# Optimization experiments

Hardware: AMD Instinct MI355X
Metric: run time of the kernel (lower is better)

Reference implementation:

```python
import jax, jax.numpy as jnp
import numpy as np

DN = ('NCHW', 'OIHW', 'NCHW')

def conv(x, w, b=None, stride=1, pad=0):
    y = jax.lax.conv_general_dilated(x, w, (stride, stride), [(pad, pad), (pad, pad)],
                                     dimension_numbers=DN)
    return y if b is None else y + b[None, :, None, None]

def conv_t(x, w, b, stride=2, pad=1):
    # PyTorch ConvTranspose2d: w is (in, out, kh, kw); equivalent to an
    # input-dilated conv with spatially flipped, in/out-swapped kernel.
    k = w.shape[2]
    w2 = jnp.flip(w, (2, 3)).transpose(1, 0, 2, 3)
    p = k - 1 - pad
    y = jax.lax.conv_general_dilated(x, w2, (1, 1), [(p, p), (p, p)],
                                     lhs_dilation=(stride, stride), dimension_numbers=DN)
    return y + b[None, :, None, None]

def res_block(x, wa, wb):
    h = conv(jax.nn.relu(x), wa, None, 1, 1)   # 3x3, no bias
    h = conv(jax.nn.relu(h), wb, None, 1, 0)   # 1x1, no bias
    return x + h

def vq(x, codebook):
    B, C, H, W = x.shape
    xf = x.transpose(0, 2, 3, 1).reshape(-1, C)                      # (N, D)
    d = ((xf * xf).sum(-1, keepdims=True)
         - 2.0 * xf @ codebook.T
         + (codebook * codebook).sum(-1)[None, :])
    idx = jnp.argmin(d, axis=1)                                      # (N,)
    q = jnp.take(codebook, idx, axis=0)                              # gather (N, D)
    return q.reshape(B, H, W, C).transpose(0, 3, 1, 2)

def setup_inputs() -> dict:
    key = jax.random.key(0)
    ks = jax.random.split(key, 16)
    r = lambda i, shape: jax.random.normal(ks[i], shape, jnp.float32) * 0.05
    K, D = 512, 64
    return {
        'x': jax.random.normal(ks[0], (32, 1, 256, 256), jnp.float32),
        'w_e1': r(1, (32, 1, 4, 4)),   'b_e1': jnp.zeros((32,), jnp.float32),
        'w_e2': r(2, (64, 32, 4, 4)),  'b_e2': jnp.zeros((64,), jnp.float32),
        'w_er1a': r(3, (32, 64, 3, 3)), 'w_er1b': r(4, (64, 32, 1, 1)),
        'w_er2a': r(5, (32, 64, 3, 3)), 'w_er2b': r(6, (64, 32, 1, 1)),
        'w_pre': r(7, (D, 64, 1, 1)),  'b_pre': jnp.zeros((D,), jnp.float32),
        'codebook': jax.random.uniform(ks[8], (K, D), jnp.float32, -1.0 / K, 1.0 / K),
        'w_d1': r(9, (64, D, 3, 3)),   'b_d1': jnp.zeros((64,), jnp.float32),
        'w_dr1a': r(10, (32, 64, 3, 3)), 'w_dr1b': r(11, (64, 32, 1, 1)),
        'w_dr2a': r(12, (32, 64, 3, 3)), 'w_dr2b': r(13, (64, 32, 1, 1)),
        'w_t1': r(14, (64, 32, 4, 4)), 'b_t1': jnp.zeros((32,), jnp.float32),
        'w_t2': r(15, (32, 1, 4, 4)),  'b_t2': jnp.zeros((1,), jnp.float32),
    }

def reference(x, w_e1, b_e1, w_e2, b_e2, w_er1a, w_er1b, w_er2a, w_er2b,
              w_pre, b_pre, codebook, w_d1, b_d1, w_dr1a, w_dr1b,
              w_dr2a, w_dr2b, w_t1, b_t1, w_t2, b_t2):
    # Encoder
    h = jax.nn.relu(conv(x, w_e1, b_e1, 2, 1))     # (B,32,128,128)
    h = conv(h, w_e2, b_e2, 2, 1)                  # (B,64,64,64)
    h = res_block(h, w_er1a, w_er1b)
    h = res_block(h, w_er2a, w_er2b)
    # pre-VQ 1x1 conv
    h = conv(h, w_pre, b_pre, 1, 0)                # (B,64,64,64)
    # Vector quantization
    q = vq(h, codebook)
    # Decoder
    d = conv(q, w_d1, b_d1, 1, 1)
    d = res_block(d, w_dr1a, w_dr1b)
    d = res_block(d, w_dr2a, w_dr2b)
    d = jax.nn.relu(conv_t(d, w_t1, b_t1))         # (B,32,128,128)
    d = conv_t(d, w_t2, b_t2)                      # (B,1,256,256)
    return d
```

## Files before the change

### kernel.cpp

```cpp
#include <hip/hip_runtime.h>
#include <hip/hip_bf16.h>


__device__ __forceinline__ float rp_elem(const float* __restrict__ src,
                                         int i, int COUT, int CIN, int KK)
{
    const int co = i % COUT;
    const int t  = i / COUT;
    const int kk = t % KK;
    const int ci = t / KK;
    return src[(co * CIN + ci) * KK + kk];
}

__global__ __launch_bounds__(256) void repack_all(
    const float* __restrict__ e1,  const float* __restrict__ e2,
    const float* __restrict__ er1a, const float* __restrict__ er1b,
    const float* __restrict__ er2a, const float* __restrict__ er2b,
    const float* __restrict__ pre, const float* __restrict__ d1,
    const float* __restrict__ dr1a, const float* __restrict__ dr1b,
    const float* __restrict__ dr2a, const float* __restrict__ dr2b,
    const float* __restrict__ t1, const float* __restrict__ cb,
    float* __restrict__ WR)
{
    const int idx = blockIdx.x * 256 + threadIdx.x;
    if (idx >= 221696) return;
    float v;
    if      (idx < 512)    v = rp_elem(e1,   idx,          32,  1, 16);
    else if (idx < 33280)  v = rp_elem(e2,   idx - 512,    64, 32, 16);
    else if (idx < 51712)  v = rp_elem(er1a, idx - 33280,  32, 64,  9);
    else if (idx < 53760)  v = rp_elem(er1b, idx - 51712,  64, 32,  1);
    else if (idx < 72192)  v = rp_elem(er2a, idx - 53760,  32, 64,  9);
    else if (idx < 74240)  v = rp_elem(er2b, idx - 72192,  64, 32,  1);
    else if (idx < 78336)  v = rp_elem(pre,  idx - 74240,  64, 64,  1);
    else if (idx < 115200) v = rp_elem(d1,   idx - 78336,  64, 64,  9);
    else if (idx < 133632) v = rp_elem(dr1a, idx - 115200, 32, 64,  9);
    else if (idx < 135680) v = rp_elem(dr1b, idx - 133632, 64, 32,  1);
    else if (idx < 154112) v = rp_elem(dr2a, idx - 135680, 32, 64,  9);
    else if (idx < 156160) v = rp_elem(dr2b, idx - 154112, 64, 32,  1);
    else if (idx < 188928) {
        const int i  = idx - 156160;
        const int co = i & 31;
        const int q  = (i >> 5) & 3;
        const int k2 = (i >> 7) & 127;
        const int pr = i >> 14;
        const int pc = q >> 1, tb = q & 1;
        const int ci = k2 >> 1, ta = k2 & 1;
        const int kh = (1 - pr) + 2 * ta, kw = (1 - pc) + 2 * tb;
        v = t1[((ci * 32 + co) * 4 + kh) * 4 + kw];
    } else {
        const int i = idx - 188928;
        const int code = i & 511;
        const int dim  = i >> 9;
        v = cb[code * 64 + dim];
    }
    WR[idx] = v;
}

__global__ __launch_bounds__(256) void vq_prep_ee(
    const float* __restrict__ cb, float* __restrict__ ee)
{
    const int k = blockIdx.x * 256 + threadIdx.x;
    const float* __restrict__ cp = cb + (size_t)k * 64;
    float s = 0.0f;
#pragma unroll
    for (int i = 0; i < 64; i++) s = fmaf(cp[i], cp[i], s);
    ee[k] = s;
}

template<int CTOT, int CPB, int CIN, int K, int S, int PAD,
         bool RELU_IN, bool HAS_BIAS, bool RESID, bool RELU_OUT>
__global__ __launch_bounds__(256) void conv_gemm(
    const float* __restrict__ in, const float* __restrict__ wr,
    const float* __restrict__ bias, const float* __restrict__ resid,
    float* __restrict__ out,
    int H, int W, int OH, int OW)
{
    constexpr int KK  = K * K;
    constexpr int CIC = (K == 1) ? 8 : 1;
    constexpr int TS  = (K == 4) ? 2 : 1;
    constexpr int KC  = CIC * KK / TS;
    constexpr int NCH = (CIN * TS) / CIC;
    constexpr int NT  = 256;
    constexpr int CPTHD = CPB / 4;
    __shared__ __align__(16) float As[2][KC * NT];

    const int tid = threadIdx.x;
    const int tpx = tid & 63;
    const int tco = __builtin_amdgcn_readfirstlane(tid >> 6);
    const int co0 = blockIdx.y * CPB + tco * CPTHD;

    const int ohow = OH * OW;
    const int n_st = blockIdx.x * NT + tid;
    const int b_st = n_st / ohow;
    const int hw_s = n_st % ohow;
    const int ih0 = (hw_s / OW) * S - PAD;
    const int iw0 = (hw_s % OW) * S - PAD;
    const float* __restrict__ inb = in + (size_t)b_st * CIN * H * W;

    float acc[CPTHD][4];
#pragma unroll
    for (int c = 0; c < CPTHD; c++) {
        const float bz = HAS_BIAS ? bias[co0 + c] : 0.0f;
#pragma unroll
        for (int q = 0; q < 4; q++) acc[c][q] = bz;
    }

    float pf[KC];
    auto stage_load = [&](int ch) {
#pragma unroll
        for (int t = 0; t < KC; t++) {
            int ci, kh, kw;
            if constexpr (K == 1) {
                ci = ch * 8 + t; kh = 0; kw = 0;
            } else if constexpr (K == 3) {
                ci = ch; kh = t / 3; kw = t % 3;
            } else {
                ci = ch >> 1;
                const int kk = ((ch & 1) << 3) + t;
                kh = kk >> 2; kw = kk & 3;
            }
            const int ih = ih0 + kh, iw = iw0 + kw;
            float v = 0.0f;
            if (ih >= 0 && ih < H && iw >= 0 && iw < W)
                v = inb[(size_t)ci * H * W + ih * W + iw];
            if (RELU_IN) v = fmaxf(v, 0.0f);
            pf[t] = v;
        }
    };

    stage_load(0);
#pragma unroll
    for (int t = 0; t < KC; t++) As[0][t * NT + tid] = pf[t];
    __syncthreads();

#pragma unroll 2
    for (int c = 0; c < NCH; c++) {
        const int cur = c & 1;
        if (c + 1 < NCH) stage_load(c + 1);

#pragma unroll
        for (int t = 0; t < KC; t++) {
            const float4 a4 = *(const float4*)(As[cur] + t * NT + tpx * 4);
            const float* __restrict__ wk =
                wr + (size_t)(c * KC + t) * CTOT + co0;
#pragma unroll
            for (int cc = 0; cc < CPTHD; cc++) {
                const float w = wk[cc];
                acc[cc][0] = fmaf(a4.x, w, acc[cc][0]);
                acc[cc][1] = fmaf(a4.y, w, acc[cc][1]);
                acc[cc][2] = fmaf(a4.z, w, acc[cc][2]);
                acc[cc][3] = fmaf(a4.w, w, acc[cc][3]);
            }
        }

        if (c + 1 < NCH) {
#pragma unroll
            for (int t = 0; t < KC; t++) As[1 - cur][t * NT + tid] = pf[t];
        }
        __syncthreads();
    }

    const int n_c  = blockIdx.x * NT + tpx * 4;
    const int b_c  = n_c / ohow;
    const int hw_c = n_c % ohow;
    float* __restrict__ op = out + (size_t)b_c * CTOT * ohow + hw_c;
    const float* __restrict__ rp =
        RESID ? (resid + (size_t)b_c * CTOT * ohow + hw_c) : nullptr;
#pragma unroll
    for (int c = 0; c < CPTHD; c++) {
        const size_t off = (size_t)(co0 + c) * ohow;
        float4 r = make_float4(acc[c][0], acc[c][1], acc[c][2], acc[c][3]);
        if (RESID) {
            const float4 rv = *(const float4*)(rp + off);
            r.x += rv.x; r.y += rv.y; r.z += rv.z; r.w += rv.w;
        }
        if (RELU_OUT) {
            r.x = fmaxf(r.x, 0.f); r.y = fmaxf(r.y, 0.f);
            r.z = fmaxf(r.z, 0.f); r.w = fmaxf(r.w, 0.f);
        }
        *(float4*)(op + off) = r;
    }
}

__global__ __launch_bounds__(512, 4) void res_tile(
    const float* __restrict__ in, const float* __restrict__ wr1,
    const float* __restrict__ wr2, float* __restrict__ out)
{
    __shared__ __align__(16) float S[13824];

    const int tid = threadIdx.x;
    const int p   = tid & 127;
    const int cog = __builtin_amdgcn_readfirstlane(tid >> 7);
    const int a   = p >> 5;
    const int c0  = (p & 31) * 2;

    const int n0   = blockIdx.x * 256;
    const int b    = n0 >> 12;
    const int row0 = (n0 & 4095) >> 6;
    const float* __restrict__ inb = in + (size_t)b * 64 * 4096;

    float4 pf4[7];
    auto stage_issue = [&](int half) {
#pragma unroll
        for (int m = 0; m < 7; m++) {
            const int f4 = m * 512 + tid;
            float4 v = make_float4(0.f, 0.f, 0.f, 0.f);
            if (f4 < 3456) {
                const int ci  = f4 / 108;
                const int rem = f4 - ci * 108;
                const int r6  = rem / 18;
                const int c4  = rem - r6 * 18;
                const int ih  = row0 + r6 - 1;
                if (ih >= 0 && ih < 64 && c4 >= 1 && c4 <= 16)
                    v = *(const float4*)(inb + (size_t)(half * 32 + ci) * 4096
                                         + ih * 64 + (c4 * 4 - 4));
            }
            pf4[m] = v;
        }
    };
    auto stage_commit = [&]() {
#pragma unroll
        for (int m = 0; m < 7; m++) {
            const int f4 = m * 512 + tid;
            if (f4 < 3456) {
                float4 v = pf4[m];
                v.x = fmaxf(v.x, 0.f); v.y = fmaxf(v.y, 0.f);
                v.z = fmaxf(v.z, 0.f); v.w = fmaxf(v.w, 0.f);
                *(float4*)(S + f4 * 4) = v;
            }
        }
    };

    const int co1 = cog * 8;
    float acc1[8][2];
#pragma unroll
    for (int c = 0; c < 8; c++) { acc1[c][0] = 0.0f; acc1[c][1] = 0.0f; }

    auto conv1_half = [&](int h) {
#pragma unroll 2
        for (int c = 0; c < 32; c++) {
            const float* __restrict__ wb =
                wr1 + (size_t)((h * 32 + c) * 9) * 32 + co1;
#pragma unroll
            for (int kh = 0; kh < 3; kh++) {
                const float* __restrict__ tp =
                    S + c * 432 + (a + kh) * 72 + 4 + c0;
                const float2 L = *(const float2*)(tp - 2);
                const float2 M = *(const float2*)(tp);
                const float2 R = *(const float2*)(tp + 2);
                const float xm = L.y;
                const float x0 = M.x;
                const float x1 = M.y;
                const float x2 = R.x;
                const float* __restrict__ wk = wb + (size_t)(kh * 3) * 32;
#pragma unroll
                for (int cc = 0; cc < 8; cc++) {
                    const float w = wk[cc];
                    acc1[cc][0] = fmaf(xm, w, acc1[cc][0]);
                    acc1[cc][1] = fmaf(x0, w, acc1[cc][1]);
                }
#pragma unroll
                for (int cc = 0; cc < 8; cc++) {
                    const float w = wk[32 + cc];
                    acc1[cc][0] = fmaf(x0, w, acc1[cc][0]);
                    acc1[cc][1] = fmaf(x1, w, acc1[cc][1]);
                }
#pragma unroll
                for (int cc = 0; cc < 8; cc++) {
                    const float w = wk[64 + cc];
                    acc1[cc][0] = fmaf(x1, w, acc1[cc][0]);
                    acc1[cc][1] = fmaf(x2, w, acc1[cc][1]);
                }
            }
        }
    };

    stage_issue(0);
    stage_commit();
    __syncthreads();
    stage_issue(1);
    conv1_half(0);
    __syncthreads();
    stage_commit();
    __syncthreads();
    conv1_half(1);
    __syncthreads();

#pragma unroll
    for (int cc = 0; cc < 8; cc++)
        *(float2*)(S + (co1 + cc) * 256 + p * 2) =
            make_float2(acc1[cc][0], acc1[cc][1]);
    __syncthreads();

    const int co2 = cog * 16;
    float acc2[16][2];
#pragma unroll
    for (int c = 0; c < 16; c++) { acc2[c][0] = 0.0f; acc2[c][1] = 0.0f; }

#pragma unroll 4
    for (int k = 0; k < 32; k++) {
        float2 m2 = *(const float2*)(S + k * 256 + p * 2);
        m2.x = fmaxf(m2.x, 0.f);
        m2.y = fmaxf(m2.y, 0.f);
        const float* __restrict__ wk = wr2 + (size_t)k * 64 + co2;
#pragma unroll
        for (int cc = 0; cc < 16; cc++) {
            const float w = wk[cc];
            acc2[cc][0] = fmaf(m2.x, w, acc2[cc][0]);
            acc2[cc][1] = fmaf(m2.y, w, acc2[cc][1]);
        }
    }

    const int hw = (n0 & 4095) + p * 2;
    const float* __restrict__ rp = inb + hw;
    float* __restrict__ op = out + (size_t)b * 64 * 4096 + hw;
#pragma unroll
    for (int cc = 0; cc < 16; cc++) {
        const size_t off = (size_t)(co2 + cc) * 4096;
        const float2 rv = *(const float2*)(rp + off);
        *(float2*)(op + off) =
            make_float2(acc2[cc][0] + rv.x, acc2[cc][1] + rv.y);
    }
}

__global__ __launch_bounds__(512, 4) void conv3_tile(
    const float* __restrict__ in, const float* __restrict__ wr,
    const float* __restrict__ bias, float* __restrict__ out)
{
    __shared__ __align__(16) float S[13824];

    const int tid = threadIdx.x;
    const int p   = tid & 127;
    const int cog = __builtin_amdgcn_readfirstlane(tid >> 7);
    const int a   = p >> 5;
    const int c0  = (p & 31) * 2;

    const int n0   = blockIdx.x * 256;
    const int b    = n0 >> 12;
    const int row0 = (n0 & 4095) >> 6;
    const float* __restrict__ inb = in + (size_t)b * 64 * 4096;

    float4 pf4[7];
    auto stage_issue = [&](int half) {
#pragma unroll
        for (int m = 0; m < 7; m++) {
            const int f4 = m * 512 + tid;
            float4 v = make_float4(0.f, 0.f, 0.f, 0.f);
            if (f4 < 3456) {
                const int ci  = f4 / 108;
                const int rem = f4 - ci * 108;
                const int r6  = rem / 18;
                const int c4  = rem - r6 * 18;
                const int ih  = row0 + r6 - 1;
                if (ih >= 0 && ih < 64 && c4 >= 1 && c4 <= 16)
                    v = *(const float4*)(inb + (size_t)(half * 32 + ci) * 4096
                                         + ih * 64 + (c4 * 4 - 4));
            }
            pf4[m] = v;
        }
    };
    auto stage_commit = [&]() {
#pragma unroll
        for (int m = 0; m < 7; m++) {
            const int f4 = m * 512 + tid;
            if (f4 < 3456) *(float4*)(S + f4 * 4) = pf4[m];
        }
    };

    const int co1 = cog * 16;
    float acc[16][2];
#pragma unroll
    for (int cc = 0; cc < 16; cc++) {
        const float bz = bias[co1 + cc];
        acc[cc][0] = bz; acc[cc][1] = bz;
    }

    auto conv_half = [&](int h) {
#pragma unroll 2
        for (int c = 0; c < 32; c++) {
            const float* __restrict__ wb =
                wr + (size_t)((h * 32 + c) * 9) * 64 + co1;
#pragma unroll
            for (int kh = 0; kh < 3; kh++) {
                const float* __restrict__ tp =
                    S + c * 432 + (a + kh) * 72 + 4 + c0;
                const float2 L = *(const float2*)(tp - 2);
                const float2 M = *(const float2*)(tp);
                const float2 R = *(const float2*)(tp + 2);
                const float xm = L.y;
                const float x0 = M.x;
                const float x1 = M.y;
                const float x2 = R.x;
                const float* __restrict__ wk = wb + (size_t)(kh * 3) * 64;
#pragma unroll
                for (int cc = 0; cc < 16; cc++) {
                    const float w = wk[cc];
                    acc[cc][0] = fmaf(xm, w, acc[cc][0]);
                    acc[cc][1] = fmaf(x0, w, acc[cc][1]);
                }
#pragma unroll
                for (int cc = 0; cc < 16; cc++) {
                    const float w = wk[64 + cc];
                    acc[cc][0] = fmaf(x0, w, acc[cc][0]);
                    acc[cc][1] = fmaf(x1, w, acc[cc][1]);
                }
#pragma unroll
                for (int cc = 0; cc < 16; cc++) {
                    const float w = wk[128 + cc];
                    acc[cc][0] = fmaf(x1, w, acc[cc][0]);
                    acc[cc][1] = fmaf(x2, w, acc[cc][1]);
                }
            }
        }
    };

    stage_issue(0);
    stage_commit();
    __syncthreads();
    stage_issue(1);
    conv_half(0);
    __syncthreads();
    stage_commit();
    __syncthreads();
    conv_half(1);

    const int hw = (n0 & 4095) + p * 2;
    float* __restrict__ op = out + (size_t)b * 64 * 4096 + hw;
#pragma unroll
    for (int cc = 0; cc < 16; cc++)
        *(float2*)(op + (size_t)(co1 + cc) * 4096) =
            make_float2(acc[cc][0], acc[cc][1]);
}

__global__ __launch_bounds__(512, 4) void conv4s2_tile(
    const float* __restrict__ in, const float* __restrict__ wr,
    const float* __restrict__ bias, float* __restrict__ out)
{
    __shared__ __align__(16) float S[13056];

    const int tid = threadIdx.x;
    const int p   = tid & 63;
    const int cog = __builtin_amdgcn_readfirstlane(tid >> 6);
    const int a   = p >> 5;
    const int c0  = (p & 31) * 2;

    const int n0   = blockIdx.x * 128;
    const int b    = n0 >> 12;
    const int row0 = (n0 & 4095) >> 6;
    const float* __restrict__ inb = in + (size_t)b * 32 * 16384;

    float4 pf4[7];
    auto stage_issue = [&](int half) {
#pragma unroll
        for (int m = 0; m < 7; m++) {
            const int f4 = m * 512 + tid;
            float4 v = make_float4(0.f, 0.f, 0.f, 0.f);
            if (f4 < 3264) {
                const int ci  = f4 / 204;
                const int rem = f4 - ci * 204;
                const int r6  = rem / 34;
                const int s   = rem - r6 * 34;
                const int ih  = 2 * row0 - 1 + r6;
                if (ih >= 0 && ih < 128 && s >= 1 && s <= 32)
                    v = *(const float4*)(inb + (size_t)(half * 16 + ci) * 16384
                                         + ih * 128 + (s - 1) * 4);
            }
            pf4[m] = v;
        }
    };
    auto stage_commit = [&]() {
#pragma unroll
        for (int m = 0; m < 7; m++) {
            const int f4 = m * 512 + tid;
            if (f4 < 3264) *(float4*)(S + f4 * 4) = pf4[m];
        }
    };

    const int co1 = cog * 8;
    float acc[8][2];
#pragma unroll
    for (int cc = 0; cc < 8; cc++) {
        const float bz = bias[co1 + cc];
        acc[cc][0] = bz; acc[cc][1] = bz;
    }

    auto conv_half = [&](int h) {
#pragma unroll 2
        for (int c = 0; c < 16; c++) {
            const float* __restrict__ wb =
                wr + (size_t)((h * 16 + c) * 16) * 64 + co1;
#pragma unroll
            for (int kh = 0; kh < 4; kh++) {
                const float* __restrict__ tp =
                    S + c * 816 + (2 * a + kh) * 136 + 2 * c0 + 2;
                const float2 E0 = *(const float2*)(tp);
                const float2 E1 = *(const float2*)(tp + 2);
                const float2 E2 = *(const float2*)(tp + 4);
                const float2 E3 = *(const float2*)(tp + 6);
                const float x0 = E0.y, x1 = E1.x, x2 = E1.y;
                const float x3 = E2.x, x4 = E2.y, x5 = E3.x;
                const float* __restrict__ wk = wb + (size_t)(kh * 4) * 64;
#pragma unroll
                for (int cc = 0; cc < 8; cc++) {
                    const float w = wk[cc];
                    acc[cc][0] = fmaf(x0, w, acc[cc][0]);
                    acc[cc][1] = fmaf(x2, w, acc[cc][1]);
                }
#pragma unroll
                for (int cc = 0; cc < 8; cc++) {
                    const float w = wk[64 + cc];
                    acc[cc][0] = fmaf(x1, w, acc[cc][0]);
                    acc[cc][1] = fmaf(x3, w, acc[cc][1]);
                }
#pragma unroll
                for (int cc = 0; cc < 8; cc++) {
                    const float w = wk[128 + cc];
                    acc[cc][0] = fmaf(x2, w, acc[cc][0]);
                    acc[cc][1] = fmaf(x4, w, acc[cc][1]);
                }
#pragma unroll
                for (int cc = 0; cc < 8; cc++) {
                    const float w = wk[192 + cc];
                    acc[cc][0] = fmaf(x3, w, acc[cc][0]);
                    acc[cc][1] = fmaf(x5, w, acc[cc][1]);
                }
            }
        }
    };

    stage_issue(0);
    stage_commit();
    __syncthreads();
    stage_issue(1);
    conv_half(0);
    __syncthreads();
    stage_commit();
    __syncthreads();
    conv_half(1);

    const int hw = (n0 & 4095) + p * 2;
    float* __restrict__ op = out + (size_t)b * 64 * 4096 + hw;
#pragma unroll
    for (int cc = 0; cc < 8; cc++)
        *(float2*)(op + (size_t)(co1 + cc) * 4096) =
            make_float2(acc[cc][0], acc[cc][1]);
}

__global__ __launch_bounds__(256) void convt_gemm2(
    const float* __restrict__ in, const float* __restrict__ wr,
    const float* __restrict__ bias, float* __restrict__ out)
{
    constexpr int NT = 256;
    __shared__ __align__(16) float As[2][12 * NT];

    const int tid = threadIdx.x;
    const int tpx = tid & 63;
    const int tco = __builtin_amdgcn_readfirstlane(tid >> 6);
    const int pr = blockIdx.y & 1;
    const int cg = blockIdx.y >> 1;
    const int co0 = cg * 16 + tco * 4;

    const int n_st = blockIdx.x * NT + tid;
    const int b = n_st >> 12;
    const int i_st = (n_st & 4095) >> 6;
    const int j_st = n_st & 63;
    const float* __restrict__ inb = in + (size_t)b * 64 * 4096;

    float acc[4][4][2];
#pragma unroll
    for (int c = 0; c < 4; c++) {
        const float bz = bias[co0 + c];
#pragma unroll
        for (int p = 0; p < 4; p++) {
            acc[c][p][0] = bz;
            acc[c][p][1] = bz;
        }
    }

    const float* __restrict__ wpr = wr + (size_t)pr * 128 * 4 * 32;

    float pf[12];
    auto stage_load = [&](int ch) {
#pragma unroll
        for (int t = 0; t < 4; t++) {
            const int k2 = ch * 4 + t;
            const int ci = k2 >> 1;
            const int ta = k2 & 1;
            const int ih = i_st + pr - ta;
            const bool rok = (ih >= 0) && (ih < 64);
            const float* __restrict__ row = inb + (size_t)ci * 4096 + ih * 64;
#pragma unroll
            for (int m = 0; m < 3; m++) {
                const int iw = j_st + m - 1;
                float v = 0.0f;
                if (rok && iw >= 0 && iw < 64) v = row[iw];
                pf[t * 3 + m] = v;
            }
        }
    };

    stage_load(0);
#pragma unroll
    for (int t = 0; t < 12; t++) As[0][t * NT + tid] = pf[t];
    __syncthreads();

#pragma unroll 2
    for (int ch = 0; ch < 32; ch++) {
        const int cur = ch & 1;
        if (ch + 1 < 32) stage_load(ch + 1);

#pragma unroll
        for (int t = 0; t < 4; t++) {
            float4 a[3];
#pragma unroll
            for (int m = 0; m < 3; m++)
                a[m] = *(const float4*)(As[cur] + (t * 3 + m) * NT + tpx * 4);
            const float* __restrict__ wk =
                wpr + (size_t)(ch * 4 + t) * 4 * 32 + co0;
#pragma unroll
            for (int tb = 0; tb < 2; tb++) {
#pragma unroll
                for (int pc = 0; pc < 2; pc++) {
                    const int q = pc * 2 + tb;
                    const int m = pc - tb + 1;
                    const float* __restrict__ wt = wk + q * 32;
                    const float vx = a[m].x, vy = a[m].y,
                                vz = a[m].z, vw = a[m].w;
#pragma unroll
                    for (int c = 0; c < 4; c++) {
                        const float w = wt[c];
                        acc[c][0][pc] = fmaf(vx, w, acc[c][0][pc]);
                        acc[c][1][pc] = fmaf(vy, w, acc[c][1][pc]);
                        acc[c][2][pc] = fmaf(vz, w, acc[c][2][pc]);
                        acc[c][3][pc] = fmaf(vw, w, acc[c][3][pc]);
                    }
                }
            }
        }

        if (ch + 1 < 32) {
#pragma unroll
            for (int t = 0; t < 12; t++) As[1 - cur][t * NT + tid] = pf[t];
        }
        __syncthreads();
    }

    const int n_c = blockIdx.x * NT + tpx * 4;
    const int i_c = (n_c & 4095) >> 6;
    const int j_c = n_c & 63;
    const int oh = 2 * i_c + pr;
    float* __restrict__ ob =
        out + (size_t)b * 32 * 16384 + (size_t)oh * 128 + 2 * j_c;
#pragma unroll
    for (int c = 0; c < 4; c++) {
        float* __restrict__ o = ob + (size_t)(co0 + c) * 16384;
        const float4 v0 = make_float4(
            fmaxf(acc[c][0][0], 0.f), fmaxf(acc[c][0][1], 0.f),
            fmaxf(acc[c][1][0], 0.f), fmaxf(acc[c][1][1], 0.f));
        const float4 v1 = make_float4(
            fmaxf(acc[c][2][0], 0.f), fmaxf(acc[c][2][1], 0.f),
            fmaxf(acc[c][3][0], 0.f), fmaxf(acc[c][3][1], 0.f));
        *(float4*)o = v0;
        *(float4*)(o + 4) = v1;
    }
}

__global__ __launch_bounds__(256) void convt2_quad(
    const float* __restrict__ in, const float* __restrict__ w,
    const float* __restrict__ bias, float* __restrict__ out, int B)
{
    const int IH = 128, IW = 128, CIN = 32, OW = 256;
    const int j = threadIdx.x & 127;
    const int i = (blockIdx.x << 1) + (threadIdx.x >> 7);
    const int b = blockIdx.y;

    const float* __restrict__ inb = in + (size_t)b * CIN * IH * IW;
    const float bz = bias[0];
    float a00 = bz, a01 = bz, a10 = bz, a11 = bz;

    const bool okm = (i > 0);
    const bool okp = (i < IH - 1);
    const bool olm = (j > 0);
    const bool olp = (j < IW - 1);

#pragma unroll 4
    for (int ci = 0; ci < CIN; ci++) {
        const float* __restrict__ p = inb + ((size_t)ci * IH + i) * IW + j;
        const float* __restrict__ wp = w + ci * 16;
        const float vmm = (okm && olm) ? p[-IW - 1] : 0.f;
        const float vm0 = okm ? p[-IW] : 0.f;
        const float vmp = (okm && olp) ? p[-IW + 1] : 0.f;
        const float v0m = olm ? p[-1] : 0.f;
        const float v00 = p[0];
        const float v0p = olp ? p[1] : 0.f;
        const float vpm = (okp && olm) ? p[IW - 1] : 0.f;
        const float vp0 = okp ? p[IW] : 0.f;
        const float vpp = (okp && olp) ? p[IW + 1] : 0.f;
        a00 = fmaf(v00, wp[1 * 4 + 1], a00);
        a00 = fmaf(v0m, wp[1 * 4 + 3], a00);
        a00 = fmaf(vm0, wp[3 * 4 + 1], a00);
        a00 = fmaf(vmm, wp[3 * 4 + 3], a00);
        a01 = fmaf(v0p, wp[1 * 4 + 0], a01);
        a01 = fmaf(v00, wp[1 * 4 + 2], a01);
        a01 = fmaf(vmp, wp[3 * 4 + 0], a01);
        a01 = fmaf(vm0, wp[3 * 4 + 2], a01);
        a10 = fmaf(vp0, wp[0 * 4 + 1], a10);
        a10 = fmaf(vpm, wp[0 * 4 + 3], a10);
        a10 = fmaf(v00, wp[2 * 4 + 1], a10);
        a10 = fmaf(v0m, wp[2 * 4 + 3], a10);
        a11 = fmaf(vpp, wp[0 * 4 + 0], a11);
        a11 = fmaf(vp0, wp[0 * 4 + 2], a11);
        a11 = fmaf(v0p, wp[2 * 4 + 0], a11);
        a11 = fmaf(v00, wp[2 * 4 + 2], a11);
    }

    float* __restrict__ outb = out + (size_t)b * 256 * 256;
    ((float2*)(outb + (size_t)(2 * i) * OW))[j] = make_float2(a00, a01);
    ((float2*)(outb + (size_t)(2 * i + 1) * OW))[j] = make_float2(a10, a11);
}

__global__ __launch_bounds__(256) void vq_gemm(
    const float* __restrict__ h,
    const float* __restrict__ cb,
    const float* __restrict__ cbT,
    const float* __restrict__ ee,
    float* __restrict__ q)
{
    __shared__ __align__(16) float As[64 * 128];
    __shared__ float xx_sh[128];
    __shared__ float pd[4 * 128];
    __shared__ int   pk[4 * 128];
    __shared__ int   bidx_sh[128];

    const int tid = threadIdx.x;
    const int tpx = tid & 63;
    const int w = __builtin_amdgcn_readfirstlane(tid >> 6);
    const int n0 = blockIdx.x * 128;
    const int b  = n0 >> 12;
    const int hw0 = n0 & 4095;

    const float* __restrict__ hb = h + (size_t)b * 64 * 4096 + hw0;
#pragma unroll
    for (int m = 0; m < 32; m++) {
        const int idx = m * 256 + tid;
        const int k = idx >> 7, p = idx & 127;
        As[idx] = hb[(size_t)k * 4096 + p];
    }
    __syncthreads();

    if (tid < 128) {
        float s = 0.0f;
#pragma unroll
        for (int i = 0; i < 64; i++) {
            const float v = As[i * 128 + tid];
            s = fmaf(v, v, s);
        }
        xx_sh[tid] = s;
    }
    __syncthreads();

    const float xx0 = xx_sh[tpx * 2];
    const float xx1 = xx_sh[tpx * 2 + 1];
    const int cwave = w * 128;

    float best0 = 3.402823466e+38f, best1 = 3.402823466e+38f;
    int bk0 = 0, bk1 = 0;

#pragma unroll 1
    for (int ch = 0; ch < 16; ch++) {
        const int cbase = cwave + ch * 8;
        float acc[8][2];
#pragma unroll
        for (int c = 0; c < 8; c++) { acc[c][0] = 0.0f; acc[c][1] = 0.0f; }

#pragma unroll 8
        for (int k = 0; k < 64; k++) {
            const float2 a2 = *(const float2*)(As + k * 128 + tpx * 2);
            const float* __restrict__ wk = cbT + (size_t)k * 512 + cbase;
#pragma unroll
            for (int c = 0; c < 8; c++) {
                const float wv = wk[c];
                acc[c][0] = fmaf(a2.x, wv, acc[c][0]);
                acc[c][1] = fmaf(a2.y, wv, acc[c][1]);
            }
        }
        const float* __restrict__ eep = ee + cbase;
#pragma unroll
        for (int c = 0; c < 8; c++) {
            const float eec = eep[c];
            const float d0 = xx0 - 2.0f * acc[c][0] + eec;
            const float d1 = xx1 - 2.0f * acc[c][1] + eec;
            if (d0 < best0) { best0 = d0; bk0 = cbase + c; }
            if (d1 < best1) { best1 = d1; bk1 = cbase + c; }
        }
    }

    pd[w * 128 + tpx * 2]     = best0;
    pd[w * 128 + tpx * 2 + 1] = best1;
    pk[w * 128 + tpx * 2]     = bk0;
    pk[w * 128 + tpx * 2 + 1] = bk1;
    __syncthreads();

    if (tid < 128) {
        float bd = pd[tid]; int bk = pk[tid];
#pragma unroll
        for (int ww = 1; ww < 4; ww++) {
            const float od = pd[ww * 128 + tid];
            if (od < bd) { bd = od; bk = pk[ww * 128 + tid]; }
        }
        bidx_sh[tid] = bk;
    }
    __syncthreads();

    {
        const int p  = tid & 127;
        const int d0 = (tid >> 7) * 32;
        const int bk = bidx_sh[p];
        const float4* __restrict__ cp4 = (const float4*)(cb + (size_t)bk * 64 + d0);
        float* __restrict__ qb = q + ((size_t)b * 64 + d0) * 4096 + hw0 + p;
#pragma unroll
        for (int i = 0; i < 8; i++) {
            const float4 v = cp4[i];
            qb[(size_t)(4 * i + 0) * 4096] = v.x;
            qb[(size_t)(4 * i + 1) * 4096] = v.y;
            qb[(size_t)(4 * i + 2) * 4096] = v.z;
            qb[(size_t)(4 * i + 3) * 4096] = v.w;
        }
    }
}

extern "C" void kernel_launch(void* const* d_in, const int* in_sizes, int n_in,
                              void* d_out, int out_size, void* d_ws, size_t ws_size,
                              hipStream_t stream) {
    const float* x      = (const float*)d_in[0];
    const float* w_e1   = (const float*)d_in[1];
    const float* b_e1   = (const float*)d_in[2];
    const float* w_e2   = (const float*)d_in[3];
    const float* b_e2   = (const float*)d_in[4];
    const float* w_er1a = (const float*)d_in[5];
    const float* w_er1b = (const float*)d_in[6];
    const float* w_er2a = (const float*)d_in[7];
    const float* w_er2b = (const float*)d_in[8];
    const float* w_pre  = (const float*)d_in[9];
    const float* b_pre  = (const float*)d_in[10];
    const float* cbk    = (const float*)d_in[11];
    const float* w_d1   = (const float*)d_in[12];
    const float* b_d1   = (const float*)d_in[13];
    const float* w_dr1a = (const float*)d_in[14];
    const float* w_dr1b = (const float*)d_in[15];
    const float* w_dr2a = (const float*)d_in[16];
    const float* w_dr2b = (const float*)d_in[17];
    const float* w_t1   = (const float*)d_in[18];
    const float* b_t1   = (const float*)d_in[19];
    const float* w_t2   = (const float*)d_in[20];
    const float* b_t2   = (const float*)d_in[21];
    float* out = (float*)d_out;

    float* A  = (float*)d_ws;
    float* Bb = A  + 16777216;
    float* C  = Bb + 8388608;
    float* D  = C  + 4194304;
    float* WR = D  + 8388608;
    float* EE = WR + 221696;

    float* r_e1  = WR;
    float* r_e2  = WR + 512;
    float* r_er1a = WR + 33280;
    float* r_er1b = WR + 51712;
    float* r_er2a = WR + 53760;
    float* r_er2b = WR + 72192;
    float* r_pre = WR + 74240;
    float* r_d1  = WR + 78336;
    float* r_dr1a = WR + 115200;
    float* r_dr1b = WR + 133632;
    float* r_dr2a = WR + 135680;
    float* r_dr2b = WR + 154112;
    float* r_t1  = WR + 156160;
    float* r_cbT = WR + 188928;

    const dim3 blk(256);
    const dim3 blk512(512);

    repack_all<<<dim3(866), blk, 0, stream>>>(
        w_e1, w_e2, w_er1a, w_er1b, w_er2a, w_er2b, w_pre, w_d1,
        w_dr1a, w_dr1b, w_dr2a, w_dr2b, w_t1, cbk, WR);
    vq_prep_ee<<<dim3(2), blk, 0, stream>>>(cbk, EE);

    conv_gemm<32, 32, 1, 4, 2, 1, false, true, false, true>
        <<<dim3(2048, 1), blk, 0, stream>>>(x, r_e1, b_e1, nullptr, A,
                                            256, 256, 128, 128);
    conv4s2_tile<<<dim3(1024), blk512, 0, stream>>>(A, r_e2, b_e2, Bb);
    res_tile<<<dim3(512), blk512, 0, stream>>>(Bb, r_er1a, r_er1b, A);
    res_tile<<<dim3(512), blk512, 0, stream>>>(A, r_er2a, r_er2b, Bb);
    conv_gemm<64, 16, 64, 1, 1, 0, false, true, false, false>
        <<<dim3(512, 4), blk, 0, stream>>>(Bb, r_pre, b_pre, nullptr, D,
                                           64, 64, 64, 64);
    vq_gemm<<<dim3(1024), blk, 0, stream>>>(D, cbk, r_cbT, EE, Bb);
    conv3_tile<<<dim3(512), blk512, 0, stream>>>(Bb, r_d1, b_d1, D);
    res_tile<<<dim3(512), blk512, 0, stream>>>(D, r_dr1a, r_dr1b, A);
    res_tile<<<dim3(512), blk512, 0, stream>>>(A, r_dr2a, r_dr2b, D);
    convt_gemm2<<<dim3(512, 4), blk, 0, stream>>>(D, r_t1, b_t1, A);
    convt2_quad<<<dim3(64, 32), blk, 0, stream>>>(A, w_t2, b_t2, out, 32);
}
```

Before: 909.3 us.

## Replace transposed-conv GEMM with smem halo-tiled kernel computing both row parities

```diff
diff --git a/kernel.cpp b/kernel.cpp
--- a/kernel.cpp
+++ b/kernel.cpp
@@ -546,122 +546,133 @@
             make_float2(acc[cc][0], acc[cc][1]);
 }
 
-__global__ __launch_bounds__(256) void convt_gemm2(
+__global__ __launch_bounds__(512, 4) void convt_tile(
     const float* __restrict__ in, const float* __restrict__ wr,
     const float* __restrict__ bias, float* __restrict__ out)
 {
-    constexpr int NT = 256;
-    __shared__ __align__(16) float As[2][12 * NT];
+    __shared__ __align__(16) float S[13824];
 
     const int tid = threadIdx.x;
-    const int tpx = tid & 63;
-    const int tco = __builtin_amdgcn_readfirstlane(tid >> 6);
-    const int pr = blockIdx.y & 1;
-    const int cg = blockIdx.y >> 1;
-    const int co0 = cg * 16 + tco * 4;
-
-    const int n_st = blockIdx.x * NT + tid;
-    const int b = n_st >> 12;
-    const int i_st = (n_st & 4095) >> 6;
-    const int j_st = n_st & 63;
+    const int p   = tid & 127;
+    const int cog = __builtin_amdgcn_readfirstlane(tid >> 7);
+    const int a   = p >> 5;
+    const int c0  = (p & 31) * 2;
+
+    const int n0   = blockIdx.x * 256;
+    const int b    = n0 >> 12;
+    const int row0 = (n0 & 4095) >> 6;
     const float* __restrict__ inb = in + (size_t)b * 64 * 4096;
 
-    float acc[4][4][2];
-#pragma unroll
-    for (int c = 0; c < 4; c++) {
-        const float bz = bias[co0 + c];
-#pragma unroll
-        for (int p = 0; p < 4; p++) {
-            acc[c][p][0] = bz;
-            acc[c][p][1] = bz;
-        }
-    }
-
-    const float* __restrict__ wpr = wr + (size_t)pr * 128 * 4 * 32;
-
-    float pf[12];
-    auto stage_load = [&](int ch) {
-#pragma unroll
-        for (int t = 0; t < 4; t++) {
-            const int k2 = ch * 4 + t;
-            const int ci = k2 >> 1;
-            const int ta = k2 & 1;
-            const int ih = i_st + pr - ta;
-            const bool rok = (ih >= 0) && (ih < 64);
-            const float* __restrict__ row = inb + (size_t)ci * 4096 + ih * 64;
-#pragma unroll
-            for (int m = 0; m < 3; m++) {
-                const int iw = j_st + m - 1;
-                float v = 0.0f;
-                if (rok && iw >= 0 && iw < 64) v = row[iw];
-                pf[t * 3 + m] = v;
-            }
-        }
-    };
-
-    stage_load(0);
-#pragma unroll
-    for (int t = 0; t < 12; t++) As[0][t * NT + tid] = pf[t];
-    __syncthreads();
-
+    float4 pf4[7];
+    auto stage_issue = [&](int half) {
+#pragma unroll
+        for (int m = 0; m < 7; m++) {
+            const int f4 = m * 512 + tid;
+            float4 v = make_float4(0.f, 0.f, 0.f, 0.f);
+            if (f4 < 3456) {
+                const int ci  = f4 / 108;
+                const int rem = f4 - ci * 108;
+                const int r6  = rem / 18;
+                const int c4  = rem - r6 * 18;
+                const int ih  = row0 + r6 - 1;
+                if (ih >= 0 && ih < 64 && c4 >= 1 && c4 <= 16)
+                    v = *(const float4*)(inb + (size_t)(half * 32 + ci) * 4096
+                                         + ih * 64 + (c4 * 4 - 4));
+            }
+            pf4[m] = v;
+        }
+    };
+    auto stage_commit = [&]() {
+#pragma unroll
+        for (int m = 0; m < 7; m++) {
+            const int f4 = m * 512 + tid;
+            if (f4 < 3456) *(float4*)(S + f4 * 4) = pf4[m];
+        }
+    };
+
+    const int co1 = cog * 8;
+    float acc[8][2][2][2];
+#pragma unroll
+    for (int cc = 0; cc < 8; cc++) {
+        const float bz = bias[co1 + cc];
+#pragma unroll
+        for (int px = 0; px < 2; px++)
+#pragma unroll
+            for (int pc = 0; pc < 2; pc++) {
+                acc[cc][px][pc][0] = bz;
+                acc[cc][px][pc][1] = bz;
+            }
+    }
+
+    auto conv_half = [&](int h) {
 #pragma unroll 2
-    for (int ch = 0; ch < 32; ch++) {
-        const int cur = ch & 1;
-        if (ch + 1 < 32) stage_load(ch + 1);
-
-#pragma unroll
-        for (int t = 0; t < 4; t++) {
-            float4 a[3];
-#pragma unroll
-            for (int m = 0; m < 3; m++)
-                a[m] = *(const float4*)(As[cur] + (t * 3 + m) * NT + tpx * 4);
-            const float* __restrict__ wk =
-                wpr + (size_t)(ch * 4 + t) * 4 * 32 + co0;
-#pragma unroll
-            for (int tb = 0; tb < 2; tb++) {
-#pragma unroll
-                for (int pc = 0; pc < 2; pc++) {
-                    const int q = pc * 2 + tb;
-                    const int m = pc - tb + 1;
-                    const float* __restrict__ wt = wk + q * 32;
-                    const float vx = a[m].x, vy = a[m].y,
-                                vz = a[m].z, vw = a[m].w;
-#pragma unroll
-                    for (int c = 0; c < 4; c++) {
-                        const float w = wt[c];
-                        acc[c][0][pc] = fmaf(vx, w, acc[c][0][pc]);
-                        acc[c][1][pc] = fmaf(vy, w, acc[c][1][pc]);
-                        acc[c][2][pc] = fmaf(vz, w, acc[c][2][pc]);
-                        acc[c][3][pc] = fmaf(vw, w, acc[c][3][pc]);
+        for (int c = 0; c < 32; c++) {
+            const int ci = h * 32 + c;
+            float X[3][4];
+#pragma unroll
+            for (int r = 0; r < 3; r++) {
+                const float* __restrict__ tp =
+                    S + c * 432 + (a + r) * 72 + 4 + c0;
+                const float2 L = *(const float2*)(tp - 2);
+                const float2 M = *(const float2*)(tp);
+                const float2 R = *(const float2*)(tp + 2);
+                X[r][0] = L.y; X[r][1] = M.x; X[r][2] = M.y; X[r][3] = R.x;
+            }
+            const float* __restrict__ wb = wr + (size_t)(ci * 2) * 128 + co1;
+#pragma unroll
+            for (int ta = 0; ta < 2; ta++) {
+                const float* X0 = X[1 - ta];
+                const float* X1 = X[2 - ta];
+                const float* __restrict__ wt = wb + ta * 128;
+#pragma unroll
+                for (int tb = 0; tb < 2; tb++) {
+#pragma unroll
+                    for (int pc = 0; pc < 2; pc++) {
+                        const int m = pc - tb + 1;
+                        const float* __restrict__ w0 = wt + (pc * 2 + tb) * 32;
+                        const float* __restrict__ w1 = w0 + 16384;
+#pragma unroll
+                        for (int cc = 0; cc < 8; cc++) {
+                            const float wv0 = w0[cc];
+                            const float wv1 = w1[cc];
+                            acc[cc][0][pc][0] =
+                                fmaf(X0[m],     wv0, acc[cc][0][pc][0]);
+                            acc[cc][1][pc][0] =
+                                fmaf(X0[m + 1], wv0, acc[cc][1][pc][0]);
+                            acc[cc][0][pc][1] =
+                                fmaf(X1[m],     wv1, acc[cc][0][pc][1]);
+                            acc[cc][1][pc][1] =
+                                fmaf(X1[m + 1], wv1, acc[cc][1][pc][1]);
+                        }
                     }
                 }
             }
         }
-
-        if (ch + 1 < 32) {
-#pragma unroll
-            for (int t = 0; t < 12; t++) As[1 - cur][t * NT + tid] = pf[t];
-        }
-        __syncthreads();
-    }
-
-    const int n_c = blockIdx.x * NT + tpx * 4;
-    const int i_c = (n_c & 4095) >> 6;
-    const int j_c = n_c & 63;
-    const int oh = 2 * i_c + pr;
+    };
+
+    stage_issue(0);
+    stage_commit();
+    __syncthreads();
+    stage_issue(1);
+    conv_half(0);
+    __syncthreads();
+    stage_commit();
+    __syncthreads();
+    conv_half(1);
+
+    const int i = row0 + a;
     float* __restrict__ ob =
-        out + (size_t)b * 32 * 16384 + (size_t)oh * 128 + 2 * j_c;
-#pragma unroll
-    for (int c = 0; c < 4; c++) {
-        float* __restrict__ o = ob + (size_t)(co0 + c) * 16384;
-        const float4 v0 = make_float4(
-            fmaxf(acc[c][0][0], 0.f), fmaxf(acc[c][0][1], 0.f),
-            fmaxf(acc[c][1][0], 0.f), fmaxf(acc[c][1][1], 0.f));
-        const float4 v1 = make_float4(
-            fmaxf(acc[c][2][0], 0.f), fmaxf(acc[c][2][1], 0.f),
-            fmaxf(acc[c][3][0], 0.f), fmaxf(acc[c][3][1], 0.f));
-        *(float4*)o = v0;
-        *(float4*)(o + 4) = v1;
+        out + (size_t)b * 32 * 16384 + (size_t)(2 * i) * 128 + 2 * c0;
+#pragma unroll
+    for (int cc = 0; cc < 8; cc++) {
+        float* __restrict__ o = ob + (size_t)(co1 + cc) * 16384;
+#pragma unroll
+        for (int pr = 0; pr < 2; pr++) {
+            const float4 v = make_float4(
+                fmaxf(acc[cc][0][0][pr], 0.f), fmaxf(acc[cc][0][1][pr], 0.f),
+                fmaxf(acc[cc][1][0][pr], 0.f), fmaxf(acc[cc][1][1][pr], 0.f));
+            *(float4*)(o + (size_t)pr * 128) = v;
+        }
     }
 }
 
@@ -899,6 +910,6 @@
     conv3_tile<<<dim3(512), blk512, 0, stream>>>(Bb, r_d1, b_d1, D);
     res_tile<<<dim3(512), blk512, 0, stream>>>(D, r_dr1a, r_dr1b, A);
     res_tile<<<dim3(512), blk512, 0, stream>>>(A, r_dr2a, r_dr2b, D);
-    convt_gemm2<<<dim3(512, 4), blk, 0, stream>>>(D, r_t1, b_t1, A);
+    convt_tile<<<dim3(512), blk512, 0, stream>>>(D, r_t1, b_t1, A);
     convt2_quad<<<dim3(64, 32), blk, 0, stream>>>(A, w_t2, b_t2, out, 32);
 }
```

Measured after the change: 896.7 us. Within noise of the previous version (-1.4%).
